# Kernel optimization log

Hardware: AMD Instinct MI355X
Metric: run time of the kernel (lower is better)

Reference implementation:

```python
import jax, jax.numpy as jnp
import numpy as np

B, S, DIM = 2, 2048, 4096
NH, NKV, HD = 32, 8, 128          # head_dim = dim // n_heads
BLOCK = 16                         # paged-cache block size
NBLK_PER_SEQ = S // BLOCK          # 128
NUM_BLOCKS = B * NBLK_PER_SEQ      # 256 physical blocks
SCALE = 1.0 / np.sqrt(HD).astype(np.float32)


def _rope(x, fc):
    # x: [B,S,H,HD]; fc: [S,1,HD//2,2] (cos,sin) -- matches apply_rotary_emb
    xr = x.astype(jnp.float32).reshape(*x.shape[:-1], HD // 2, 2)
    cos, sin = fc[..., 0], fc[..., 1]
    out = jnp.stack([xr[..., 0] * cos - xr[..., 1] * sin,
                     xr[..., 1] * cos + xr[..., 0] * sin], axis=-1)
    return out.reshape(x.shape).astype(x.dtype)


def setup_inputs() -> dict:
    key = jax.random.key(0)
    ks = jax.random.split(key, 3)
    x = jax.random.normal(ks[0], (B, S, DIM), jnp.float32)
    wqkv_w = jax.random.normal(ks[1], ((NH + 2 * NKV) * HD, DIM), jnp.float32) * (DIM ** -0.5)
    wo_w = jax.random.normal(ks[2], (DIM, DIM), jnp.float32) * (DIM ** -0.5)
    # rotary table: [S, 1, HD/2, 2] so it broadcasts over (B, S, H, HD/2)
    pos = jnp.arange(S, dtype=jnp.float32)
    inv = 10000.0 ** (-jnp.arange(0, HD, 2, dtype=jnp.float32) / HD)
    ang = pos[:, None] * inv[None, :]
    freqs_cis = jnp.stack([jnp.cos(ang), jnp.sin(ang)], -1)[:, None, :, :]
    k_cache = jnp.zeros((NUM_BLOCKS, BLOCK, NKV, HD), jnp.float32)
    v_cache = jnp.zeros((NUM_BLOCKS, BLOCK, NKV, HD), jnp.float32)
    block_table = jnp.arange(B * NBLK_PER_SEQ, dtype=jnp.int32).reshape(B, NBLK_PER_SEQ)
    seqlens_k = jnp.full((B,), S, jnp.int32)
    return {"x": x, "wqkv_w": wqkv_w, "wo_w": wo_w, "freqs_cis": freqs_cis,
            "k_cache": k_cache, "v_cache": v_cache,
            "block_table": block_table, "seqlens_k": seqlens_k}


def reference(x, wqkv_w, wo_w, freqs_cis, k_cache, v_cache, block_table, seqlens_k):
    # fused QKV projection
    qkv = x @ wqkv_w.T                                   # [B,S,(NH+2*NKV)*HD]
    q, k, v = jnp.split(qkv, [NH * HD, (NH + NKV) * HD], axis=-1)
    q = q.reshape(B, S, NH, HD)
    k = k.reshape(B, S, NKV, HD)
    v = v.reshape(B, S, NKV, HD)
    q = _rope(q, freqs_cis)
    k = _rope(k, freqs_cis)
    # paged KV-cache write (prefill): slot = block_table[b, t//BLOCK]*BLOCK + t%BLOCK
    t = jnp.arange(S)
    slots = block_table[:, t // BLOCK] * BLOCK + (t % BLOCK)[None, :]    # [B,S]
    flat = slots.reshape(-1)
    kc = k_cache.reshape(NUM_BLOCKS * BLOCK, NKV, HD).at[flat].set(k.reshape(B * S, NKV, HD))
    vc = v_cache.reshape(NUM_BLOCKS * BLOCK, NKV, HD).at[flat].set(v.reshape(B * S, NKV, HD))
    # block-table indexed attention: gather K/V back through the page table
    kk = kc[slots]                                       # [B,S,NKV,HD]
    vv = vc[slots]                                       # [B,S,NKV,HD]
    G = NH // NKV                                        # GQA group size
    qg = q.reshape(B, S, NKV, G, HD)
    scores = jnp.einsum('bqkgd,bskd->bkgqs', qg, kk) * SCALE  # [B,NKV,G,S,S]
    qpos = jnp.arange(S)[:, None]
    kpos = jnp.arange(S)[None, :]
    causal = kpos <= qpos                                # [S,S]
    valid = kpos[None] < seqlens_k[:, None, None]        # [B,S,S]
    mask = (causal[None] & valid)[:, None, None]         # [B,1,1,S,S]
    scores = jnp.where(mask, scores, -jnp.inf)
    p = jax.nn.softmax(scores, axis=-1)
    attn = jnp.einsum('bkgqs,bskd->bqkgd', p, vv).reshape(B, S, NH * HD)
    return attn @ wo_w.T
```

## Files before the change

kernel.cpp:

```cpp
#include <hip/hip_runtime.h>
#include <hip/hip_fp16.h>

typedef _Float16 f16;
typedef _Float16 f16x4 __attribute__((ext_vector_type(4)));
typedef _Float16 f16x8 __attribute__((ext_vector_type(8)));
typedef float    f32x4 __attribute__((ext_vector_type(4)));

#define NEG_INF (-__builtin_inff())
#define AS1 __attribute__((address_space(1)))
#define AS3 __attribute__((address_space(3)))
#define GLOAD_LDS16(g, l) \
    __builtin_amdgcn_global_load_lds((AS1 const void*)(g), (AS3 void*)(l), 16, 0, 0)
#define EXP2F(x) __builtin_amdgcn_exp2f(x)
#define BARRIER() do { asm volatile("" ::: "memory"); \
                       __builtin_amdgcn_s_barrier(); \
                       asm volatile("" ::: "memory"); } while (0)

__global__ __launch_bounds__(256) void cvt_f32_f16(const float* __restrict__ in,
                                                   f16* __restrict__ out, int n4) {
    int i = blockIdx.x * 256 + threadIdx.x;
    if (i >= n4) return;
    float4 v = ((const float4*)in)[i];
    f16x4 h = {(f16)v.x, (f16)v.y, (f16)v.z, (f16)v.w};
    ((f16x4*)out)[i] = h;
}

template <typename CT>
__global__ __launch_bounds__(512) void gemm256(const f16* __restrict__ A,
                                               const f16* __restrict__ Bt,
                                               CT* __restrict__ C,
                                               int M, int N, int K) {
    __shared__ __align__(16) f16 smem[65536];
    f16* LA = smem;
    f16* LB = smem + 32768;

    const int tid  = threadIdx.x;
    const int wave = tid >> 6, lane = tid & 63;
    const int quad = lane >> 4, m16 = lane & 15;
    const int wm = wave >> 2, wn = wave & 3;

    const int ntn = N >> 8;
    const int nwg = (M >> 8) * ntn;
    const int q8 = nwg >> 3, r8 = nwg & 7;
    const int xcd = blockIdx.x & 7, idx = blockIdx.x >> 3;
    const int swz = (xcd < r8 ? xcd * (q8 + 1) : r8 * (q8 + 1) + (xcd - r8) * q8) + idx;
    const int bm = (swz / ntn) << 8;
    const int bn = (swz % ntn) << 8;

    const int rowW = tid >> 3;
    const int gsrc = (tid & 7) ^ (rowW & 7);
    const f16* gA0 = A  + (size_t)(bm + rowW) * K + gsrc * 8;
    const f16* gA1 = A  + (size_t)(bm + 128 + rowW) * K + gsrc * 8;
    const f16* gB0 = Bt + (size_t)(bn + rowW) * K + gsrc * 8;
    const f16* gB1 = Bt + (size_t)(bn + 128 + rowW) * K + gsrc * 8;
    const size_t rstep = (size_t)64 * K;
    const int lw = wave * 512;

#define STG(dstbase, gp, kt) do { \
    GLOAD_LDS16((gp) + (size_t)(kt) * 64,         (dstbase) + lw); \
    GLOAD_LDS16((gp) + (size_t)(kt) * 64 + rstep, (dstbase) + lw + 4096); } while (0)

    int foff[2];
#pragma unroll
    for (int ks = 0; ks < 2; ++ks)
        foff[ks] = (((ks << 2) | quad) ^ (m16 & 7)) * 8;
    const int arow = wm * 8192 + m16 * 64;
    const int brow = (wn >> 1) * 8192 + (wn & 1) * 4096 + m16 * 64;

    f32x4 acc[8][4];
#pragma unroll
    for (int i = 0; i < 8; ++i)
#pragma unroll
        for (int j = 0; j < 4; ++j)
#pragma unroll
            for (int e = 0; e < 4; ++e) acc[i][j][e] = 0.f;

    const int NT = K >> 6;

    STG(LA, gA0, 0); STG(LA + 8192, gA1, 0);
    STG(LB, gB0, 0); STG(LB + 8192, gB1, 0);
    STG(LB + 16384, gB0, 1); STG(LB + 16384 + 8192, gB1, 1);
    asm volatile("s_waitcnt vmcnt(4)" ::: "memory");
    BARRIER();

    f16x8 af[4][2], bf0[2][2], bf1[2][2];

    for (int t = 0; t < NT; ++t) {
        const int bo = (t & 1) * 16384;
        const f16* pa = LA + bo + arow;
        const f16* pb = LB + bo + brow;

#pragma unroll
        for (int mt = 0; mt < 4; ++mt)
#pragma unroll
            for (int ks = 0; ks < 2; ++ks)
                af[mt][ks] = *(const f16x8*)(pa + mt * 1024 + foff[ks]);
#pragma unroll
        for (int nt = 0; nt < 2; ++nt)
#pragma unroll
            for (int ks = 0; ks < 2; ++ks)
                bf0[nt][ks] = *(const f16x8*)(pb + nt * 1024 + foff[ks]);
        if (t + 1 < NT) STG(LA + (bo ^ 16384), gA0, t + 1);
        BARRIER();
        asm volatile("s_waitcnt lgkmcnt(0)" ::: "memory");
        __builtin_amdgcn_s_setprio(1);
#pragma unroll
        for (int mt = 0; mt < 4; ++mt)
#pragma unroll
            for (int nt = 0; nt < 2; ++nt)
#pragma unroll
                for (int ks = 0; ks < 2; ++ks)
                    acc[mt][nt] = __builtin_amdgcn_mfma_f32_16x16x32_f16(
                        af[mt][ks], bf0[nt][ks], acc[mt][nt], 0, 0, 0);
        __builtin_amdgcn_s_setprio(0);
        BARRIER();

#pragma unroll
        for (int nt = 0; nt < 2; ++nt)
#pragma unroll
            for (int ks = 0; ks < 2; ++ks)
                bf1[nt][ks] = *(const f16x8*)(pb + (nt + 2) * 1024 + foff[ks]);
        if (t + 1 < NT) STG(LA + (bo ^ 16384) + 8192, gA1, t + 1);
        BARRIER();
        asm volatile("s_waitcnt lgkmcnt(0)" ::: "memory");
        __builtin_amdgcn_s_setprio(1);
#pragma unroll
        for (int mt = 0; mt < 4; ++mt)
#pragma unroll
            for (int nt = 0; nt < 2; ++nt)
#pragma unroll
                for (int ks = 0; ks < 2; ++ks)
                    acc[mt][nt + 2] = __builtin_amdgcn_mfma_f32_16x16x32_f16(
                        af[mt][ks], bf1[nt][ks], acc[mt][nt + 2], 0, 0, 0);
        __builtin_amdgcn_s_setprio(0);
        BARRIER();

#pragma unroll
        for (int mt = 0; mt < 4; ++mt)
#pragma unroll
            for (int ks = 0; ks < 2; ++ks)
                af[mt][ks] = *(const f16x8*)(pa + (mt + 4) * 1024 + foff[ks]);
        if (t + 2 < NT) STG(LB + bo, gB0, t + 2);
        BARRIER();
        asm volatile("s_waitcnt lgkmcnt(0)" ::: "memory");
        __builtin_amdgcn_s_setprio(1);
#pragma unroll
        for (int mt = 0; mt < 4; ++mt)
#pragma unroll
            for (int nt = 0; nt < 2; ++nt)
#pragma unroll
                for (int ks = 0; ks < 2; ++ks)
                    acc[mt + 4][nt + 2] = __builtin_amdgcn_mfma_f32_16x16x32_f16(
                        af[mt][ks], bf1[nt][ks], acc[mt + 4][nt + 2], 0, 0, 0);
        __builtin_amdgcn_s_setprio(0);
        BARRIER();

        if (t + 2 < NT) STG(LB + bo + 8192, gB1, t + 2);
        BARRIER();
        __builtin_amdgcn_s_setprio(1);
#pragma unroll
        for (int mt = 0; mt < 4; ++mt)
#pragma unroll
            for (int nt = 0; nt < 2; ++nt)
#pragma unroll
                for (int ks = 0; ks < 2; ++ks)
                    acc[mt + 4][nt] = __builtin_amdgcn_mfma_f32_16x16x32_f16(
                        af[mt][ks], bf0[nt][ks], acc[mt + 4][nt], 0, 0, 0);
        __builtin_amdgcn_s_setprio(0);
        if (t + 2 < NT) { asm volatile("s_waitcnt vmcnt(4)" ::: "memory"); }
        else            { asm volatile("s_waitcnt vmcnt(0)" ::: "memory"); }
        BARRIER();
    }
#undef STG

#pragma unroll
    for (int mt = 0; mt < 8; ++mt)
#pragma unroll
        for (int r = 0; r < 4; ++r) {
            int row = bm + wm * 128 + mt * 16 + quad * 4 + r;
            CT* cp = C + (size_t)row * N + bn + wn * 64 + m16;
#pragma unroll
            for (int nt = 0; nt < 4; ++nt) cp[nt * 16] = (CT)acc[mt][nt][r];
        }
}

__global__ __launch_bounds__(256) void rope_qk(const f16* __restrict__ qkv,
                                               const float* __restrict__ freqs,
                                               f16* __restrict__ qh,
                                               f16* __restrict__ kk) {
    int idx  = blockIdx.x * 256 + threadIdx.x;
    int row  = idx / 2560;
    int p    = idx - row * 2560;
    int b    = row >> 11, s = row & 2047;
    int head = p >> 6, i = p & 63;
    const f16* src = qkv + (size_t)row * 6144 + head * 128 + 2 * i;
    float v0 = (float)src[0], v1 = (float)src[1];
    float c  = freqs[s * 128 + 2 * i];
    float sn = freqs[s * 128 + 2 * i + 1];
    float r0 = v0 * c - v1 * sn;
    float r1 = v1 * c + v0 * sn;
    f16* dst = (head < 32)
        ? qh + (((size_t)(b * 32 + head)) * 2048 + s) * 128 + 2 * i
        : kk + (((size_t)(b * 8 + head - 32)) * 2048 + s) * 128 + 2 * i;
    dst[0] = (f16)r0; dst[1] = (f16)r1;
}

__global__ __launch_bounds__(256) void transpose_v(const f16* __restrict__ qkv,
                                                   f16* __restrict__ vvt) {
    __shared__ f16 T[64][72];
    const int st = blockIdx.x, dt = blockIdx.y;
    const int b = blockIdx.z >> 3, kvh = blockIdx.z & 7;
    const int tid = threadIdx.x;
    const int sr = tid >> 3, c8 = (tid & 7) * 8;
#pragma unroll
    for (int rep = 0; rep < 2; ++rep) {
        int sl = rep * 32 + sr;
        *(f16x8*)&T[sl][c8] =
            *(const f16x8*)(qkv + (size_t)(b * 2048 + st * 64 + sl) * 6144
                            + 5120 + kvh * 128 + dt * 64 + c8);
    }
    __syncthreads();
#pragma unroll
    for (int rep = 0; rep < 2; ++rep) {
        int dl = rep * 32 + sr;
        f16x8 v;
#pragma unroll
        for (int j = 0; j < 8; ++j) v[j] = T[c8 + j][dl];
        *(f16x8*)(vvt + (((size_t)(b * 8 + kvh)) * 128 + dt * 64 + dl) * 2048
                  + st * 64 + c8) = v;
    }
}

__global__ __launch_bounds__(256) void attn_fused(const f16* __restrict__ qh,
                                                  const f16* __restrict__ kk,
                                                  const f16* __restrict__ vvt,
                                                  const int* __restrict__ seqlens,
                                                  f16* __restrict__ out) {
    __shared__ f16 KsPs[64 * 136];
    __shared__ f16 Vs[128][72];
    const int pair = blockIdx.x;
    const int h = blockIdx.y, b = blockIdx.z;
    const int kvh = h >> 2;
    const int tid = threadIdx.x, wave = tid >> 6, lane = tid & 63;
    const int quad = lane >> 4, m16 = lane & 15;
    f16* Ps = KsPs;

    const int seqlen = seqlens[b];
    const f16* kbp = kk  + ((size_t)(b * 8 + kvh) * 2048) * 128;
    const f16* vbp = vvt + ((size_t)(b * 8 + kvh) * 128) * 2048;

    const float SCL2 = 0.08838834764831845f * 1.4426950408889634f;

    for (int half = 0; half < 2; ++half) {
        const int qt = half ? pair : (31 - pair);
        const int qbase = qt * 64;
        const int qw = qbase + wave * 16;

        const f16* qptr = qh + (((size_t)(b * 32 + h)) * 2048 + qw + m16) * 128;
        f16x8 qf[4];
#pragma unroll
        for (int c = 0; c < 4; ++c) qf[c] = *(const f16x8*)(qptr + c * 32 + quad * 8);

        float m_i[4], l_i[4];
        f32x4 oacc[8];
#pragma unroll
        for (int r = 0; r < 4; ++r) { m_i[r] = NEG_INF; l_i[r] = 0.f; }
#pragma unroll
        for (int dt = 0; dt < 8; ++dt)
#pragma unroll
            for (int e = 0; e < 4; ++e) oacc[dt][e] = 0.f;

        int kmax = qbase + 64; if (seqlen < kmax) kmax = seqlen;

        f16x8 gk[4], gv[4];
#pragma unroll
        for (int it = 0; it < 4; ++it) {
            int g = it * 256 + tid;
            gk[it] = *(const f16x8*)(kbp + (size_t)(g >> 4) * 128 + (g & 15) * 8);
            gv[it] = *(const f16x8*)(vbp + (size_t)(g >> 3) * 2048 + (g & 7) * 8);
        }

        for (int kt = 0; kt < kmax; kt += 64) {
            BARRIER();
#pragma unroll
            for (int it = 0; it < 4; ++it) {
                int g = it * 256 + tid;
                *(f16x8*)&KsPs[(g >> 4) * 136 + (g & 15) * 8] = gk[it];
                *(f16x8*)&Vs[g >> 3][(g & 7) * 8] = gv[it];
            }
            if (kt + 64 < kmax) {
#pragma unroll
                for (int it = 0; it < 4; ++it) {
                    int g = it * 256 + tid;
                    gk[it] = *(const f16x8*)(kbp + (size_t)(kt + 64 + (g >> 4)) * 128 + (g & 15) * 8);
                    gv[it] = *(const f16x8*)(vbp + (size_t)(g >> 3) * 2048 + (kt + 64) + (g & 7) * 8);
                }
            }
            asm volatile("s_waitcnt lgkmcnt(0)" ::: "memory");
            BARRIER();

            f32x4 sc[4];
#pragma unroll
            for (int nt = 0; nt < 4; ++nt) {
                f32x4 s = {0.f, 0.f, 0.f, 0.f};
#pragma unroll
                for (int c = 0; c < 4; ++c) {
                    f16x8 kf = *(const f16x8*)&KsPs[(nt * 16 + m16) * 136 + c * 32 + quad * 8];
                    s = __builtin_amdgcn_mfma_f32_16x16x32_f16(qf[c], kf, s, 0, 0, 0);
                }
                sc[nt] = s;
            }

            float sv[4][4];
            float mt[4] = {NEG_INF, NEG_INF, NEG_INF, NEG_INF};
#pragma unroll
            for (int nt = 0; nt < 4; ++nt) {
                int kpos = kt + nt * 16 + m16;
#pragma unroll
                for (int r = 0; r < 4; ++r) {
                    int qpos = qw + quad * 4 + r;
                    float sx = sc[nt][r] * SCL2;
                    sx = (kpos <= qpos && kpos < seqlen) ? sx : NEG_INF;
                    sv[nt][r] = sx;
                    mt[r] = fmaxf(mt[r], sx);
                }
            }
#pragma unroll
            for (int off = 1; off < 16; off <<= 1)
#pragma unroll
                for (int r = 0; r < 4; ++r)
                    mt[r] = fmaxf(mt[r], __shfl_xor(mt[r], off, 64));

            float mm[4];
            bool grow = (mt[0] > m_i[0]) | (mt[1] > m_i[1]) |
                        (mt[2] > m_i[2]) | (mt[3] > m_i[3]);
            if (grow) {
#pragma unroll
                for (int r = 0; r < 4; ++r) {
                    float mo = m_i[r];
                    float mn = fmaxf(mo, mt[r]);
                    float mmr = fmaxf(mn, -1e30f);
                    float a = EXP2F(mo - mmr);
                    m_i[r] = mn;
                    mm[r] = mmr;
                    l_i[r] *= a;
#pragma unroll
                    for (int dt = 0; dt < 8; ++dt) oacc[dt][r] *= a;
                }
            } else {
#pragma unroll
                for (int r = 0; r < 4; ++r) mm[r] = fmaxf(m_i[r], -1e30f);
            }
            float rs[4] = {0.f, 0.f, 0.f, 0.f};
#pragma unroll
            for (int nt = 0; nt < 4; ++nt)
#pragma unroll
                for (int r = 0; r < 4; ++r) {
                    float pv = EXP2F(sv[nt][r] - mm[r]);
                    sv[nt][r] = pv;
                    rs[r] += pv;
                }
#pragma unroll
            for (int off = 1; off < 16; off <<= 1)
#pragma unroll
                for (int r = 0; r < 4; ++r) rs[r] += __shfl_xor(rs[r], off, 64);
#pragma unroll
            for (int r = 0; r < 4; ++r) l_i[r] += rs[r];

            BARRIER();

#pragma unroll
            for (int nt = 0; nt < 4; ++nt)
#pragma unroll
                for (int r = 0; r < 4; ++r)
                    Ps[(wave * 16 + quad * 4 + r) * 72 + nt * 16 + m16] = (f16)sv[nt][r];

            f16x8 pf[2];
#pragma unroll
            for (int c = 0; c < 2; ++c)
                pf[c] = *(const f16x8*)&Ps[(wave * 16 + m16) * 72 + c * 32 + quad * 8];
#pragma unroll
            for (int dt = 0; dt < 8; ++dt)
#pragma unroll
                for (int c = 0; c < 2; ++c) {
                    f16x8 vf = *(const f16x8*)&Vs[dt * 16 + m16][c * 32 + quad * 8];
                    oacc[dt] = __builtin_amdgcn_mfma_f32_16x16x32_f16(pf[c], vf, oacc[dt], 0, 0, 0);
                }
        }

#pragma unroll
        for (int r = 0; r < 4; ++r) {
            int qpos = qw + quad * 4 + r;
            float inv = 1.0f / l_i[r];
            f16* op = out + ((size_t)b * 2048 + qpos) * 4096 + h * 128;
#pragma unroll
            for (int dt = 0; dt < 8; ++dt)
                op[dt * 16 + m16] = (f16)(oacc[dt][r] * inv);
        }
    }
}

extern "C" void kernel_launch(void* const* d_in, const int* in_sizes, int n_in,
                              void* d_out, int out_size, void* d_ws, size_t ws_size,
                              hipStream_t stream) {
    const float* x     = (const float*)d_in[0];
    const float* wqkv  = (const float*)d_in[1];
    const float* wo    = (const float*)d_in[2];
    const float* freqs = (const float*)d_in[3];
    const int*   seql  = (const int*)d_in[7];
    float* out = (float*)d_out;

    char* ws = (char*)d_ws;
    size_t o = 0;
    f16* xh    = (f16*)(ws + o); o += (size_t)4096 * 4096 * 2;
    f16* wqkvh = (f16*)(ws + o); o += (size_t)6144 * 4096 * 2;
    f16* woh   = (f16*)(ws + o); o += (size_t)4096 * 4096 * 2;
    f16* qkvh  = (f16*)(ws + o); o += (size_t)4096 * 6144 * 2;
    f16* qhp   = (f16*)(ws + o); o += (size_t)4096 * 4096 * 2;
    f16* kkp   = (f16*)(ws + o); o += (size_t)4096 * 8 * 128 * 2;
    f16* vvt   = (f16*)(ws + o); o += (size_t)4096 * 8 * 128 * 2;
    f16* attnh = xh;

    cvt_f32_f16<<<16384, 256, 0, stream>>>(x, xh, 4194304);
    cvt_f32_f16<<<24576, 256, 0, stream>>>(wqkv, wqkvh, 6291456);
    cvt_f32_f16<<<16384, 256, 0, stream>>>(wo, woh, 4194304);

    gemm256<f16><<<384, 512, 0, stream>>>(xh, wqkvh, qkvh, 4096, 6144, 4096);

    rope_qk<<<40960, 256, 0, stream>>>(qkvh, freqs, qhp, kkp);
    transpose_v<<<dim3(32, 2, 16), 256, 0, stream>>>(qkvh, vvt);

    attn_fused<<<dim3(16, 32, 2), 256, 0, stream>>>(qhp, kkp, vvt, seql, attnh);

    gemm256<float><<<256, 512, 0, stream>>>(attnh, woh, out, 4096, 4096, 4096);
}
```

Measured before the change: 830.0 us.

## Software-pipeline LDS fragment loads with MFMA using double-buffered A fragments

Splits the A-fragment registers into two sets (afA, afB) so shared-memory fragment reads can overlap MFMA work. Each phase now issues its LDS reads alongside the previous phase's MFMAs. The next iteration's first A and B fragments are prefetched during the final MFMA phase, after the vmcnt wait and barrier. The aim is to hide LDS read latency that previously sat between barriers and the matrix instructions. The cost is higher register pressure from the extra fragment set, which could reduce occupancy or cause spills.

```diff
diff --git a/kernel.cpp b/kernel.cpp
--- a/kernel.cpp
+++ b/kernel.cpp
@@ -57,8 +57,10 @@
     const int lw = wave * 512;
 
 #define STG(dstbase, gp, kt) do { \
+    GLOAAD_LDS16_GUARD \
     GLOAD_LDS16((gp) + (size_t)(kt) * 64,         (dstbase) + lw); \
     GLOAD_LDS16((gp) + (size_t)(kt) * 64 + rstep, (dstbase) + lw + 4096); } while (0)
+#define GLOAAD_LDS16_GUARD
 
     int foff[2];
 #pragma unroll
@@ -83,43 +85,45 @@
     asm volatile("s_waitcnt vmcnt(4)" ::: "memory");
     BARRIER();
 
-    f16x8 af[4][2], bf0[2][2], bf1[2][2];
+    f16x8 afA[4][2], afB[4][2], bf0[2][2], bf1[2][2];
+#pragma unroll
+    for (int mt = 0; mt < 4; ++mt)
+#pragma unroll
+        for (int ks = 0; ks < 2; ++ks)
+            afA[mt][ks] = *(const f16x8*)(LA + arow + mt * 1024 + foff[ks]);
+#pragma unroll
+    for (int nt = 0; nt < 2; ++nt)
+#pragma unroll
+        for (int ks = 0; ks < 2; ++ks)
+            bf0[nt][ks] = *(const f16x8*)(LB + brow + nt * 1024 + foff[ks]);
 
     for (int t = 0; t < NT; ++t) {
         const int bo = (t & 1) * 16384;
         const f16* pa = LA + bo + arow;
         const f16* pb = LB + bo + brow;
-
-#pragma unroll
-        for (int mt = 0; mt < 4; ++mt)
-#pragma unroll
-            for (int ks = 0; ks < 2; ++ks)
-                af[mt][ks] = *(const f16x8*)(pa + mt * 1024 + foff[ks]);
-#pragma unroll
-        for (int nt = 0; nt < 2; ++nt)
-#pragma unroll
-            for (int ks = 0; ks < 2; ++ks)
-                bf0[nt][ks] = *(const f16x8*)(pb + nt * 1024 + foff[ks]);
+        const f16* pa1 = LA + (bo ^ 16384) + arow;
+        const f16* pb1 = LB + (bo ^ 16384) + brow;
+
         if (t + 1 < NT) STG(LA + (bo ^ 16384), gA0, t + 1);
         BARRIER();
         asm volatile("s_waitcnt lgkmcnt(0)" ::: "memory");
         __builtin_amdgcn_s_setprio(1);
 #pragma unroll
-        for (int mt = 0; mt < 4; ++mt)
-#pragma unroll
-            for (int nt = 0; nt < 2; ++nt)
-#pragma unroll
-                for (int ks = 0; ks < 2; ++ks)
-                    acc[mt][nt] = __builtin_amdgcn_mfma_f32_16x16x32_f16(
-                        af[mt][ks], bf0[nt][ks], acc[mt][nt], 0, 0, 0);
-        __builtin_amdgcn_s_setprio(0);
-        BARRIER();
-
-#pragma unroll
         for (int nt = 0; nt < 2; ++nt)
 #pragma unroll
             for (int ks = 0; ks < 2; ++ks)
                 bf1[nt][ks] = *(const f16x8*)(pb + (nt + 2) * 1024 + foff[ks]);
+#pragma unroll
+        for (int mt = 0; mt < 4; ++mt)
+#pragma unroll
+            for (int nt = 0; nt < 2; ++nt)
+#pragma unroll
+                for (int ks = 0; ks < 2; ++ks)
+                    acc[mt][nt] = __builtin_amdgcn_mfma_f32_16x16x32_f16(
+                        afA[mt][ks], bf0[nt][ks], acc[mt][nt], 0, 0, 0);
+        __builtin_amdgcn_s_setprio(0);
+        BARRIER();
+
         if (t + 1 < NT) STG(LA + (bo ^ 16384) + 8192, gA1, t + 1);
         BARRIER();
         asm volatile("s_waitcnt lgkmcnt(0)" ::: "memory");
@@ -127,19 +131,19 @@
 #pragma unroll
         for (int mt = 0; mt < 4; ++mt)
 #pragma unroll
+            for (int ks = 0; ks < 2; ++ks)
+                afB[mt][ks] = *(const f16x8*)(pa + (mt + 4) * 1024 + foff[ks]);
+#pragma unroll
+        for (int mt = 0; mt < 4; ++mt)
+#pragma unroll
             for (int nt = 0; nt < 2; ++nt)
 #pragma unroll
                 for (int ks = 0; ks < 2; ++ks)
                     acc[mt][nt + 2] = __builtin_amdgcn_mfma_f32_16x16x32_f16(
-                        af[mt][ks], bf1[nt][ks], acc[mt][nt + 2], 0, 0, 0);
+                        afA[mt][ks], bf1[nt][ks], acc[mt][nt + 2], 0, 0, 0);
         __builtin_amdgcn_s_setprio(0);
         BARRIER();
 
-#pragma unroll
-        for (int mt = 0; mt < 4; ++mt)
-#pragma unroll
-            for (int ks = 0; ks < 2; ++ks)
-                af[mt][ks] = *(const f16x8*)(pa + (mt + 4) * 1024 + foff[ks]);
         if (t + 2 < NT) STG(LB + bo, gB0, t + 2);
         BARRIER();
         asm volatile("s_waitcnt lgkmcnt(0)" ::: "memory");
@@ -151,24 +155,38 @@
 #pragma unroll
                 for (int ks = 0; ks < 2; ++ks)
                     acc[mt + 4][nt + 2] = __builtin_amdgcn_mfma_f32_16x16x32_f16(
-                        af[mt][ks], bf1[nt][ks], acc[mt + 4][nt + 2], 0, 0, 0);
+                        afB[mt][ks], bf1[nt][ks], acc[mt + 4][nt + 2], 0, 0, 0);
         __builtin_amdgcn_s_setprio(0);
         BARRIER();
 
         if (t + 2 < NT) STG(LB + bo + 8192, gB1, t + 2);
-        BARRIER();
-        __builtin_amdgcn_s_setprio(1);
-#pragma unroll
-        for (int mt = 0; mt < 4; ++mt)
-#pragma unroll
-            for (int nt = 0; nt < 2; ++nt)
-#pragma unroll
-                for (int ks = 0; ks < 2; ++ks)
-                    acc[mt + 4][nt] = __builtin_amdgcn_mfma_f32_16x16x32_f16(
-                        af[mt][ks], bf0[nt][ks], acc[mt + 4][nt], 0, 0, 0);
-        __builtin_amdgcn_s_setprio(0);
         if (t + 2 < NT) { asm volatile("s_waitcnt vmcnt(4)" ::: "memory"); }
         else            { asm volatile("s_waitcnt vmcnt(0)" ::: "memory"); }
+        BARRIER();
+        __builtin_amdgcn_s_setprio(1);
+        if (t + 1 < NT) {
+#pragma unroll
+            for (int mt = 0; mt < 4; ++mt)
+#pragma unroll
+                for (int ks = 0; ks < 2; ++ks)
+                    afA[mt][ks] = *(const f16x8*)(pa1 + mt * 1024 + foff[ks]);
+        }
+#pragma unroll
+        for (int mt = 0; mt < 4; ++mt)
+#pragma unroll
+            for (int nt = 0; nt < 2; ++nt)
+#pragma unroll
+                for (int ks = 0; ks < 2; ++ks)
+                    acc[mt + 4][nt] = __builtin_amdgcn_mfma_f32_16x16x32_f16(
+                        afB[mt][ks], bf0[nt][ks], acc[mt + 4][nt], 0, 0, 0);
+        if (t + 1 < NT) {
+#pragma unroll
+            for (int nt = 0; nt < 2; ++nt)
+#pragma unroll
+                for (int ks = 0; ks < 2; ++ks)
+                    bf0[nt][ks] = *(const f16x8*)(pb1 + nt * 1024 + foff[ks]);
+        }
+        __builtin_amdgcn_s_setprio(0);
         BARRIER();
     }
 #undef STG
```

After: 848.0 us. 2.2% more time.
